# Performance work log

Measured on AMD Instinct MI355X. Metric: run time of the kernel, lower is better.

The kernel has to match this reference:

```python
import jax, jax.numpy as jnp
import numpy as np

B, H, S, DK = 2, 16, 2048, 64

def setup_inputs() -> dict:
    key = jax.random.key(0)
    kq, kk, kv, km = jax.random.split(key, 4)
    queries = jax.random.normal(kq, (B, H, S, DK), dtype=jnp.float32)
    keys = jax.random.normal(kk, (B, H, S, DK), dtype=jnp.float32)
    values = jax.random.normal(kv, (B, H, S, DK), dtype=jnp.float32)
    mask = jax.random.randint(km, (B, S, S), 0, 2, dtype=jnp.int32)
    return {"queries": queries, "keys": keys, "values": values, "mask": mask}

def reference(queries, keys, values, mask):
    d_k = queries.shape[-1]
    scale = 1.0 / np.sqrt(d_k).astype(np.float32)
    # [B,H,S,S]
    scores = jnp.einsum('bhqd,bhkd->bhqk', queries, keys) * scale
    m = mask[:, None, :, :]  # broadcast over heads, like mask.unsqueeze(1)
    scores = jnp.where(m == 0, jnp.asarray(-1e9, scores.dtype), scores)
    attn = jax.nn.softmax(scores, axis=-1)
    return jnp.einsum('bhqk,bhkd->bhqd', attn, values)
```

## Files before the change

kernel.cpp:

```cpp
#include <hip/hip_runtime.h>


#define S_   2048
#define D_   64
#define H_   16
#define B_   2
#define BH_  32
#define KVB  64
#define NKV  (S_/KVB)
#define QPB  128
#define NQT  (S_/QPB)

#define KSCALE 0.18033688f

typedef __attribute__((ext_vector_type(8))) _Float16 f16x8;
typedef __attribute__((ext_vector_type(4))) _Float16 f16x4;
typedef __attribute__((ext_vector_type(2))) _Float16 f16x2;
typedef __attribute__((ext_vector_type(4))) float    f32x4;

static __device__ __forceinline__ void async16(const void* g, void* l) {
  __builtin_amdgcn_global_load_lds(
      (const __attribute__((address_space(1))) void*)g,
      (__attribute__((address_space(3))) void*)l, 16, 0, 0);
}

static __device__ __forceinline__ f16x2 pkrtz(float a, float b) {
  return __builtin_bit_cast(f16x2, __builtin_amdgcn_cvt_pkrtz(a, b));
}

__global__ __launch_bounds__(256) void prepass_k(
    const float* __restrict__ K, const float* __restrict__ V,
    const int* __restrict__ M,
    _Float16* __restrict__ Kh, _Float16* __restrict__ Vth,
    unsigned long long* __restrict__ Mb) {
  __shared__ float tile[64][65];
  const int bidx = blockIdx.x;
  const int tid = threadIdx.x;
  if (bidx < 1024) {
    int st = bidx & 31;
    int bh = bidx >> 5;
    const float* src = V + ((size_t)bh * S_ + st * 64) * D_;
    int r = tid >> 2, cq = tid & 3;
#pragma unroll
    for (int j = 0; j < 4; ++j) {
      float4 v = ((const float4*)(src + (size_t)r * D_))[cq + 4 * j];
      int col = (cq + 4 * j) * 4;
      tile[r][col + 0] = v.x; tile[r][col + 1] = v.y;
      tile[r][col + 2] = v.z; tile[r][col + 3] = v.w;
    }
    __syncthreads();
    int d = tid >> 2, s = (tid & 3) * 16;
    _Float16 tmp[16];
#pragma unroll
    for (int j = 0; j < 16; ++j) tmp[j] = (_Float16)tile[s + j][d];
    _Float16* dstp = Vth + ((size_t)bh * D_ + d) * S_ + st * 64 + s;
    *(f16x8*)(dstp)     = *((f16x8*)tmp);
    *(f16x8*)(dstp + 8) = *((f16x8*)tmp + 1);
  } else if (bidx < 1536) {
    int idx = (bidx - 1024) * 256 + tid;
#pragma unroll
    for (int j = 0; j < 8; ++j) {
      int i = idx + j * 131072;
      float4 v = ((const float4*)K)[i];
      f16x4 o = {(_Float16)(v.x * KSCALE), (_Float16)(v.y * KSCALE),
                 (_Float16)(v.z * KSCALE), (_Float16)(v.w * KSCALE)};
      *(f16x4*)(Kh + 4 * (size_t)i) = o;
    }
  } else {
    int lane = tid & 63;
    int wb = (bidx - 1536) * 256 + (tid >> 6) * 64;
    for (int i = 0; i < 64; ++i) {
      int w = wb + i;
      int m = M[(size_t)w * 64 + lane];
      unsigned long long bal = __ballot(m != 0);
      if (lane == 0) Mb[w] = bal;
    }
  }
}

__global__ __launch_bounds__(512, 6) void attn_fwd(
    const float* __restrict__ Qf, const _Float16* __restrict__ Kh,
    const _Float16* __restrict__ Vth, const unsigned long long* __restrict__ Mb,
    float* __restrict__ Out) {
  __shared__ _Float16 Kt[2][KVB * D_];
  __shared__ _Float16 Vt[2][D_ * KVB];
  __shared__ _Float16 Pl[8][16 * KVB];
  __shared__ unsigned long long MLUT[16];

  const int tid = threadIdx.x;
  const int lane = tid & 63;
  const int wid = tid >> 6;
  const int g = lane >> 4;
  const int c = lane & 15;
  const int c7 = c & 7;

  if (tid < 16) {
    unsigned w0 = ((tid & 1) ? 0x3C00u : 0u) | ((tid & 2) ? 0x3C000000u : 0u);
    unsigned w1 = ((tid & 4) ? 0x3C00u : 0u) | ((tid & 8) ? 0x3C000000u : 0u);
    MLUT[tid] = (unsigned long long)w0 | ((unsigned long long)w1 << 32);
  }

  int bid = blockIdx.x;
  bid = (bid & 7) * 64 + (bid >> 3);
  const int qt = bid & (NQT - 1);
  const int bh = bid >> 4;
  const int b = bh >> 4;

  const int q0 = qt * QPB + wid * 16;

  f16x8 qf[2];
  {
    const float* qp = Qf + ((size_t)bh * S_ + q0 + c) * D_ + 8 * g;
    _Float16 t[16];
#pragma unroll
    for (int j = 0; j < 8; ++j) t[j] = (_Float16)qp[j];
#pragma unroll
    for (int j = 0; j < 8; ++j) t[8 + j] = (_Float16)qp[32 + j];
    qf[0] = *(f16x8*)t;
    qf[1] = *((f16x8*)t + 1);
  }

  f32x4 accO[4];
#pragma unroll
  for (int dp = 0; dp < 4; ++dp) accO[dp] = {0.f, 0.f, 0.f, 0.f};
  float m_run = -INFINITY, l_run = 0.f;

  const int srow = tid >> 3, sgr = tid & 7;
  const _Float16* kp0 = Kh + (size_t)bh * S_ * D_ + (size_t)srow * D_ + ((sgr ^ (srow & 7)) << 3);
  const _Float16* vp0 = Vth + (size_t)bh * D_ * S_ + (size_t)srow * S_ + ((sgr ^ (srow & 7)) << 3);
  _Float16* ldk = &Kt[0][(tid & ~63) * 8];
  _Float16* ldv = &Vt[0][(tid & ~63) * 8];
  const unsigned long long* pmb = Mb + ((size_t)b * S_ + q0 + c) * NKV;

  const f16x2 one2 = {(_Float16)1.0f, (_Float16)1.0f};

  async16(kp0, ldk);
  async16(vp0, ldv);

#pragma unroll 2
  for (int kv = 0; kv < NKV; ++kv) {
    const int cur = kv & 1;
    __syncthreads();

    unsigned long long mw = pmb[kv];

    if (kv + 1 < NKV) {
      const int nxt = cur ^ 1;
      async16(kp0 + (size_t)(kv + 1) * (KVB * D_), ldk + nxt * (KVB * D_));
      async16(vp0 + (size_t)(kv + 1) * KVB,        ldv + nxt * (D_ * KVB));
    }

    const _Float16* Ktc = Kt[cur];
    const _Float16* Vtc = Vt[cur];

    f32x4 st[4];
    __builtin_amdgcn_s_setprio(1);
#pragma unroll
    for (int kt = 0; kt < 4; ++kt) {
      int row = kt * 16 + c;
      f16x8 k0 = *(const f16x8*)(&Ktc[row * D_ + (((0 * 4 + g) ^ c7) << 3)]);
      f16x8 k1 = *(const f16x8*)(&Ktc[row * D_ + (((1 * 4 + g) ^ c7) << 3)]);
      f32x4 a = {0.f, 0.f, 0.f, 0.f};
      a = __builtin_amdgcn_mfma_f32_16x16x32_f16(k0, qf[0], a, 0, 0, 0);
      a = __builtin_amdgcn_mfma_f32_16x16x32_f16(k1, qf[1], a, 0, 0, 0);
      st[kt] = a;
    }
    __builtin_amdgcn_s_setprio(0);

    float pmax = st[0][0];
#pragma unroll
    for (int kt = 0; kt < 4; ++kt)
#pragma unroll
      for (int r = 0; r < 4; ++r) pmax = fmaxf(pmax, st[kt][r]);
    pmax = fmaxf(pmax, __shfl_xor(pmax, 16));
    pmax = fmaxf(pmax, __shfl_xor(pmax, 32));
    if (!__all(pmax - m_run <= 8.f)) {
      float mn = fmaxf(m_run, pmax);
      float cf = __builtin_amdgcn_exp2f(m_run - mn);
      l_run *= cf;
#pragma unroll
      for (int dp = 0; dp < 4; ++dp) accO[dp] = accO[dp] * cf;
      m_run = mn;
    }

    const unsigned mlo = (unsigned)mw, mhi = (unsigned)(mw >> 32);
    float rs = 0.f;
    f16x2 wv[8];
#pragma unroll
    for (int kt = 0; kt < 4; ++kt) {
      unsigned nib = (((kt < 2) ? mlo : mhi) >> (((kt & 1) << 4) + 4 * g)) & 0xFu;
      unsigned long long lut = MLUT[nib];
      f16x2 m01 = __builtin_bit_cast(f16x2, (unsigned)lut);
      f16x2 m23 = __builtin_bit_cast(f16x2, (unsigned)(lut >> 32));
      f16x2 p01 = pkrtz(__builtin_amdgcn_exp2f(st[kt][0] - m_run),
                        __builtin_amdgcn_exp2f(st[kt][1] - m_run));
      f16x2 p23 = pkrtz(__builtin_amdgcn_exp2f(st[kt][2] - m_run),
                        __builtin_amdgcn_exp2f(st[kt][3] - m_run));
      wv[2 * kt]     = p01 * m01;
      wv[2 * kt + 1] = p23 * m23;
      rs = __builtin_amdgcn_fdot2(wv[2 * kt], one2, rs, false);
      rs = __builtin_amdgcn_fdot2(wv[2 * kt + 1], one2, rs, false);
    }
    rs += __shfl_xor(rs, 16);
    rs += __shfl_xor(rs, 32);
    l_run += rs;

    _Float16* pw = Pl[wid] + c * KVB;
#pragma unroll
    for (int kt = 0; kt < 4; ++kt) {
      int gp = (2 * kt + (g >> 1)) ^ c7;
      uint2 wpair = {__builtin_bit_cast(unsigned, wv[2 * kt]),
                     __builtin_bit_cast(unsigned, wv[2 * kt + 1])};
      *(uint2*)(pw + gp * 8 + (g & 1) * 4) = wpair;
    }
    asm volatile("s_waitcnt lgkmcnt(0)" ::: "memory");
    __builtin_amdgcn_sched_barrier(0);

    __builtin_amdgcn_s_setprio(1);
#pragma unroll
    for (int ks = 0; ks < 2; ++ks) {
      const _Float16* pr = Pl[wid] + c * KVB + (((4 * ks + g) ^ c7) << 3);
      f16x8 pf = *(const f16x8*)pr;
#pragma unroll
      for (int dp = 0; dp < 4; ++dp) {
        int row = dp * 16 + c;
        f16x8 vfr = *(const f16x8*)(&Vtc[row * KVB + (((4 * ks + g) ^ c7) << 3)]);
        accO[dp] = __builtin_amdgcn_mfma_f32_16x16x32_f16(vfr, pf, accO[dp], 0, 0, 0);
      }
    }
    __builtin_amdgcn_s_setprio(0);
  }

  float inv = 1.0f / l_run;
  float* op = Out + ((size_t)bh * S_ + q0 + c) * D_;
#pragma unroll
  for (int dp = 0; dp < 4; ++dp) {
    f32x4 o = accO[dp] * inv;
    *(f32x4*)(op + dp * 16 + 4 * g) = o;
  }
}

extern "C" void kernel_launch(void* const* d_in, const int* in_sizes, int n_in,
                              void* d_out, int out_size, void* d_ws, size_t ws_size,
                              hipStream_t stream) {
  const float* Q = (const float*)d_in[0];
  const float* K = (const float*)d_in[1];
  const float* V = (const float*)d_in[2];
  const int*   M = (const int*)d_in[3];
  float* Out = (float*)d_out;

  const size_t NE = (size_t)B_ * H_ * S_ * D_;
  _Float16* Kh  = (_Float16*)d_ws;
  _Float16* Vth = Kh + NE;
  unsigned long long* Mb = (unsigned long long*)(Vth + NE);

  prepass_k<<<2048, 256, 0, stream>>>(K, V, M, Kh, Vth, Mb);
  attn_fwd<<<NQT * BH_, 512, 0, stream>>>(Q, Kh, Vth, Mb, Out);
}
```

Measured before the change: 195.0 us.

## Switch attention to 32x32x16 MFMA with register-resident P via permlane swap

Moves the attention kernel from 16x16x32 MFMAs to 32x32x16 MFMAs, with each wave now owning 32 query rows and the block shrinking to 4 waves of 256 threads. The P matrix is no longer written to and re-read from LDS. It is rearranged in registers with permlane32_swap, or a shuffle fallback, to form the B operand of the PV MFMA. The aim is to remove the LDS round-trip and waitcnt stall for P and to raise MFMA efficiency per instruction. The cost is more accumulator registers per lane, fewer waves per block, and lower occupancy.

```diff
diff --git a/kernel.cpp b/kernel.cpp
--- a/kernel.cpp
+++ b/kernel.cpp
@@ -13,10 +13,12 @@
 
 #define KSCALE 0.18033688f
 
-typedef __attribute__((ext_vector_type(8))) _Float16 f16x8;
-typedef __attribute__((ext_vector_type(4))) _Float16 f16x4;
-typedef __attribute__((ext_vector_type(2))) _Float16 f16x2;
-typedef __attribute__((ext_vector_type(4))) float    f32x4;
+typedef __attribute__((ext_vector_type(8)))  _Float16 f16x8;
+typedef __attribute__((ext_vector_type(4)))  _Float16 f16x4;
+typedef __attribute__((ext_vector_type(2)))  _Float16 f16x2;
+typedef __attribute__((ext_vector_type(4)))  float    f32x4;
+typedef __attribute__((ext_vector_type(16))) float    f32x16;
+typedef __attribute__((ext_vector_type(4)))  unsigned u32x4;
 
 static __device__ __forceinline__ void async16(const void* g, void* l) {
   __builtin_amdgcn_global_load_lds(
@@ -26,6 +28,18 @@
 
 static __device__ __forceinline__ f16x2 pkrtz(float a, float b) {
   return __builtin_bit_cast(f16x2, __builtin_amdgcn_cvt_pkrtz(a, b));
+}
+
+static __device__ __forceinline__ void plswap(unsigned& a, unsigned& b, int h) {
+#if __has_builtin(__builtin_amdgcn_permlane32_swap)
+  auto r = __builtin_amdgcn_permlane32_swap(a, b, false, false);
+  a = (unsigned)r[0];
+  b = (unsigned)r[1];
+#else
+  unsigned sa = __shfl_xor(a, 32), sb = __shfl_xor(b, 32);
+  unsigned na = h ? sb : a, nb = h ? b : sa;
+  a = na; b = nb;
+#endif
 }
 
 __global__ __launch_bounds__(256) void prepass_k(
@@ -78,21 +92,20 @@
   }
 }
 
-__global__ __launch_bounds__(512, 6) void attn_fwd(
+__global__ __launch_bounds__(256, 2) void attn_fwd(
     const float* __restrict__ Qf, const _Float16* __restrict__ Kh,
     const _Float16* __restrict__ Vth, const unsigned long long* __restrict__ Mb,
     float* __restrict__ Out) {
   __shared__ _Float16 Kt[2][KVB * D_];
   __shared__ _Float16 Vt[2][D_ * KVB];
-  __shared__ _Float16 Pl[8][16 * KVB];
   __shared__ unsigned long long MLUT[16];
 
   const int tid = threadIdx.x;
   const int lane = tid & 63;
   const int wid = tid >> 6;
-  const int g = lane >> 4;
-  const int c = lane & 15;
-  const int c7 = c & 7;
+  const int h = lane >> 5;
+  const int c5 = lane & 31;
+  const int c7 = c5 & 7;
 
   if (tid < 16) {
     unsigned w0 = ((tid & 1) ? 0x3C00u : 0u) | ((tid & 2) ? 0x3C000000u : 0u);
@@ -106,137 +119,146 @@
   const int bh = bid >> 4;
   const int b = bh >> 4;
 
-  const int q0 = qt * QPB + wid * 16;
-
-  f16x8 qf[2];
+  const int q = qt * QPB + wid * 32 + c5;
+
+  f16x8 qf[4];
   {
-    const float* qp = Qf + ((size_t)bh * S_ + q0 + c) * D_ + 8 * g;
-    _Float16 t[16];
-#pragma unroll
-    for (int j = 0; j < 8; ++j) t[j] = (_Float16)qp[j];
-#pragma unroll
-    for (int j = 0; j < 8; ++j) t[8 + j] = (_Float16)qp[32 + j];
-    qf[0] = *(f16x8*)t;
-    qf[1] = *((f16x8*)t + 1);
-  }
-
-  f32x4 accO[4];
-#pragma unroll
-  for (int dp = 0; dp < 4; ++dp) accO[dp] = {0.f, 0.f, 0.f, 0.f};
+    const float* qp = Qf + ((size_t)bh * S_ + q) * D_ + 8 * h;
+#pragma unroll
+    for (int dc = 0; dc < 4; ++dc) {
+      _Float16 t[8];
+#pragma unroll
+      for (int j = 0; j < 8; ++j) t[j] = (_Float16)qp[16 * dc + j];
+      qf[dc] = *(f16x8*)t;
+    }
+  }
+
+  f32x16 accO0, accO1;
+#pragma unroll
+  for (int e = 0; e < 16; ++e) { accO0[e] = 0.f; accO1[e] = 0.f; }
   float m_run = -INFINITY, l_run = 0.f;
 
-  const int srow = tid >> 3, sgr = tid & 7;
-  const _Float16* kp0 = Kh + (size_t)bh * S_ * D_ + (size_t)srow * D_ + ((sgr ^ (srow & 7)) << 3);
-  const _Float16* vp0 = Vth + (size_t)bh * D_ * S_ + (size_t)srow * S_ + ((sgr ^ (srow & 7)) << 3);
-  _Float16* ldk = &Kt[0][(tid & ~63) * 8];
-  _Float16* ldv = &Vt[0][(tid & ~63) * 8];
-  const unsigned long long* pmb = Mb + ((size_t)b * S_ + q0 + c) * NKV;
-
+  const _Float16* kbase = Kh + (size_t)bh * S_ * D_;
+  const _Float16* vbase = Vth + (size_t)bh * D_ * S_;
+  const unsigned long long* pmb = Mb + ((size_t)b * S_ + q) * NKV;
   const f16x2 one2 = {(_Float16)1.0f, (_Float16)1.0f};
 
-  async16(kp0, ldk);
-  async16(vp0, ldv);
+#define STAGE(buf, kvi)                                                     \
+  {                                                                         \
+    _Pragma("unroll") for (int it = 0; it < 2; ++it) {                      \
+      int gid = it * 256 + tid;                                             \
+      int row = gid >> 3, gr = gid & 7;                                     \
+      int gs = (gr ^ (row & 7)) << 3;                                       \
+      int ldso = ((gid & ~63) * 8);                                         \
+      async16(kbase + ((size_t)((kvi)*KVB + row)) * D_ + gs, &Kt[buf][ldso]); \
+      async16(vbase + (size_t)row * S_ + (kvi)*KVB + gs, &Vt[buf][ldso]);   \
+    }                                                                       \
+  }
+
+  STAGE(0, 0);
 
 #pragma unroll 2
   for (int kv = 0; kv < NKV; ++kv) {
     const int cur = kv & 1;
     __syncthreads();
-
     unsigned long long mw = pmb[kv];
-
-    if (kv + 1 < NKV) {
-      const int nxt = cur ^ 1;
-      async16(kp0 + (size_t)(kv + 1) * (KVB * D_), ldk + nxt * (KVB * D_));
-      async16(vp0 + (size_t)(kv + 1) * KVB,        ldv + nxt * (D_ * KVB));
-    }
+    if (kv + 1 < NKV) STAGE(cur ^ 1, kv + 1);
 
     const _Float16* Ktc = Kt[cur];
     const _Float16* Vtc = Vt[cur];
 
-    f32x4 st[4];
+    f32x16 st0, st1;
+#pragma unroll
+    for (int e = 0; e < 16; ++e) { st0[e] = 0.f; st1[e] = 0.f; }
     __builtin_amdgcn_s_setprio(1);
 #pragma unroll
-    for (int kt = 0; kt < 4; ++kt) {
-      int row = kt * 16 + c;
-      f16x8 k0 = *(const f16x8*)(&Ktc[row * D_ + (((0 * 4 + g) ^ c7) << 3)]);
-      f16x8 k1 = *(const f16x8*)(&Ktc[row * D_ + (((1 * 4 + g) ^ c7) << 3)]);
-      f32x4 a = {0.f, 0.f, 0.f, 0.f};
-      a = __builtin_amdgcn_mfma_f32_16x16x32_f16(k0, qf[0], a, 0, 0, 0);
-      a = __builtin_amdgcn_mfma_f32_16x16x32_f16(k1, qf[1], a, 0, 0, 0);
-      st[kt] = a;
+    for (int dc = 0; dc < 4; ++dc) {
+      int slot = (((2 * dc + h) ^ c7) << 3);
+      f16x8 k0 = *(const f16x8*)(&Ktc[(c5)      * D_ + slot]);
+      f16x8 k1 = *(const f16x8*)(&Ktc[(32 + c5) * D_ + slot]);
+      st0 = __builtin_amdgcn_mfma_f32_32x32x16_f16(k0, qf[dc], st0, 0, 0, 0);
+      st1 = __builtin_amdgcn_mfma_f32_32x32x16_f16(k1, qf[dc], st1, 0, 0, 0);
     }
     __builtin_amdgcn_s_setprio(0);
 
-    float pmax = st[0][0];
-#pragma unroll
-    for (int kt = 0; kt < 4; ++kt)
-#pragma unroll
-      for (int r = 0; r < 4; ++r) pmax = fmaxf(pmax, st[kt][r]);
-    pmax = fmaxf(pmax, __shfl_xor(pmax, 16));
+    float pmax = -INFINITY;
+#pragma unroll
+    for (int e = 0; e < 16; ++e) {
+      pmax = fmaxf(pmax, st0[e]);
+      pmax = fmaxf(pmax, st1[e]);
+    }
     pmax = fmaxf(pmax, __shfl_xor(pmax, 32));
     if (!__all(pmax - m_run <= 8.f)) {
       float mn = fmaxf(m_run, pmax);
       float cf = __builtin_amdgcn_exp2f(m_run - mn);
       l_run *= cf;
 #pragma unroll
-      for (int dp = 0; dp < 4; ++dp) accO[dp] = accO[dp] * cf;
+      for (int e = 0; e < 16; ++e) { accO0[e] *= cf; accO1[e] *= cf; }
       m_run = mn;
     }
 
-    const unsigned mlo = (unsigned)mw, mhi = (unsigned)(mw >> 32);
     float rs = 0.f;
-    f16x2 wv[8];
-#pragma unroll
-    for (int kt = 0; kt < 4; ++kt) {
-      unsigned nib = (((kt < 2) ? mlo : mhi) >> (((kt & 1) << 4) + 4 * g)) & 0xFu;
-      unsigned long long lut = MLUT[nib];
-      f16x2 m01 = __builtin_bit_cast(f16x2, (unsigned)lut);
-      f16x2 m23 = __builtin_bit_cast(f16x2, (unsigned)(lut >> 32));
-      f16x2 p01 = pkrtz(__builtin_amdgcn_exp2f(st[kt][0] - m_run),
-                        __builtin_amdgcn_exp2f(st[kt][1] - m_run));
-      f16x2 p23 = pkrtz(__builtin_amdgcn_exp2f(st[kt][2] - m_run),
-                        __builtin_amdgcn_exp2f(st[kt][3] - m_run));
-      wv[2 * kt]     = p01 * m01;
-      wv[2 * kt + 1] = p23 * m23;
-      rs = __builtin_amdgcn_fdot2(wv[2 * kt], one2, rs, false);
-      rs = __builtin_amdgcn_fdot2(wv[2 * kt + 1], one2, rs, false);
-    }
-    rs += __shfl_xor(rs, 16);
+    unsigned pkd[2][4][2];
+#pragma unroll
+    for (int kt = 0; kt < 2; ++kt) {
+#pragma unroll
+      for (int rr = 0; rr < 4; ++rr) {
+        int n = 8 * kt + 2 * rr + h;
+        unsigned nib = (unsigned)(mw >> (4 * n)) & 0xFu;
+        unsigned long long lut = MLUT[nib];
+        f16x2 m01 = __builtin_bit_cast(f16x2, (unsigned)lut);
+        f16x2 m23 = __builtin_bit_cast(f16x2, (unsigned)(lut >> 32));
+        float e0 = (kt ? st1[4 * rr + 0] : st0[4 * rr + 0]) - m_run;
+        float e1 = (kt ? st1[4 * rr + 1] : st0[4 * rr + 1]) - m_run;
+        float e2 = (kt ? st1[4 * rr + 2] : st0[4 * rr + 2]) - m_run;
+        float e3 = (kt ? st1[4 * rr + 3] : st0[4 * rr + 3]) - m_run;
+        f16x2 p0 = pkrtz(__builtin_amdgcn_exp2f(e0), __builtin_amdgcn_exp2f(e1)) * m01;
+        f16x2 p1 = pkrtz(__builtin_amdgcn_exp2f(e2), __builtin_amdgcn_exp2f(e3)) * m23;
+        rs = __builtin_amdgcn_fdot2(p0, one2, rs, false);
+        rs = __builtin_amdgcn_fdot2(p1, one2, rs, false);
+        pkd[kt][rr][0] = __builtin_bit_cast(unsigned, p0);
+        pkd[kt][rr][1] = __builtin_bit_cast(unsigned, p1);
+      }
+    }
     rs += __shfl_xor(rs, 32);
     l_run += rs;
 
-    _Float16* pw = Pl[wid] + c * KVB;
-#pragma unroll
-    for (int kt = 0; kt < 4; ++kt) {
-      int gp = (2 * kt + (g >> 1)) ^ c7;
-      uint2 wpair = {__builtin_bit_cast(unsigned, wv[2 * kt]),
-                     __builtin_bit_cast(unsigned, wv[2 * kt + 1])};
-      *(uint2*)(pw + gp * 8 + (g & 1) * 4) = wpair;
-    }
-    asm volatile("s_waitcnt lgkmcnt(0)" ::: "memory");
-    __builtin_amdgcn_sched_barrier(0);
+    f16x8 pfrag[4];
+#pragma unroll
+    for (int kc = 0; kc < 4; ++kc) {
+      int jl = 2 * kc, jh = 2 * kc + 1;
+      unsigned a0 = pkd[jl >> 2][jl & 3][0], a1 = pkd[jl >> 2][jl & 3][1];
+      unsigned b0 = pkd[jh >> 2][jh & 3][0], b1 = pkd[jh >> 2][jh & 3][1];
+      plswap(a0, b0, h);
+      plswap(a1, b1, h);
+      u32x4 fr = {a0, a1, b0, b1};
+      pfrag[kc] = __builtin_bit_cast(f16x8, fr);
+    }
 
     __builtin_amdgcn_s_setprio(1);
 #pragma unroll
-    for (int ks = 0; ks < 2; ++ks) {
-      const _Float16* pr = Pl[wid] + c * KVB + (((4 * ks + g) ^ c7) << 3);
-      f16x8 pf = *(const f16x8*)pr;
-#pragma unroll
-      for (int dp = 0; dp < 4; ++dp) {
-        int row = dp * 16 + c;
-        f16x8 vfr = *(const f16x8*)(&Vtc[row * KVB + (((4 * ks + g) ^ c7) << 3)]);
-        accO[dp] = __builtin_amdgcn_mfma_f32_16x16x32_f16(vfr, pf, accO[dp], 0, 0, 0);
-      }
+    for (int kc = 0; kc < 4; ++kc) {
+      int slot = (((2 * kc + h) ^ c7) << 3);
+      f16x8 v0 = *(const f16x8*)(&Vtc[(c5)      * KVB + slot]);
+      f16x8 v1 = *(const f16x8*)(&Vtc[(32 + c5) * KVB + slot]);
+      accO0 = __builtin_amdgcn_mfma_f32_32x32x16_f16(v0, pfrag[kc], accO0, 0, 0, 0);
+      accO1 = __builtin_amdgcn_mfma_f32_32x32x16_f16(v1, pfrag[kc], accO1, 0, 0, 0);
     }
     __builtin_amdgcn_s_setprio(0);
   }
 
   float inv = 1.0f / l_run;
-  float* op = Out + ((size_t)bh * S_ + q0 + c) * D_;
-#pragma unroll
-  for (int dp = 0; dp < 4; ++dp) {
-    f32x4 o = accO[dp] * inv;
-    *(f32x4*)(op + dp * 16 + 4 * g) = o;
+  float* op = Out + ((size_t)bh * S_ + q) * D_;
+#pragma unroll
+  for (int rr = 0; rr < 4; ++rr) {
+    f32x4 o0, o1;
+#pragma unroll
+    for (int e = 0; e < 4; ++e) {
+      o0[e] = accO0[4 * rr + e] * inv;
+      o1[e] = accO1[4 * rr + e] * inv;
+    }
+    *(f32x4*)(op + 8 * rr + 4 * h)      = o0;
+    *(f32x4*)(op + 32 + 8 * rr + 4 * h) = o1;
   }
 }
 
@@ -255,5 +277,5 @@
   unsigned long long* Mb = (unsigned long long*)(Vth + NE);
 
   prepass_k<<<2048, 256, 0, stream>>>(K, V, M, Kh, Vth, Mb);
-  attn_fwd<<<NQT * BH_, 512, 0, stream>>>(Q, Kh, Vth, Mb, Out);
-}
+  attn_fwd<<<NQT * BH_, 256, 0, stream>>>(Q, Kh, Vth, Mb, Out);
+}
```

New measurement: 192.6 us. Within noise of the previous version (-1.2%).
